# Optimization experiments

Hardware: AMD Instinct MI355X
Metric: run time of the kernel (lower is better)

## Reference

```python
import jax, jax.numpy as jnp
import numpy as np
from jax import lax

K = 3        # kernel_size
PAD = 1      # padding
DIL = 1      # dilation
C_IN = 64
C_OUT = 64
B, H, W = 8, 128, 128


def conv2d(x, w, b, pad):
    # x: [n,c,h,w], w: [o,i,kh,kw], pad: (ph, pw)
    out = lax.conv_general_dilated(
        x, w, window_strides=(1, 1),
        padding=[(pad[0], pad[0]), (pad[1], pad[1])],
        rhs_dilation=(DIL, DIL),
        dimension_numbers=("NCHW", "OIHW", "NCHW"))
    return out + b[None, :, None, None]


def bilinear_sample(x, py, px):
    # x: [n,c,h,w]; py/px: [n,K,h,w] fractional sample coords (zeros outside).
    n, c, h, w = x.shape
    y0 = jnp.floor(py)
    x0 = jnp.floor(px)
    wy = py - y0  # frac weights
    wx = px - x0
    xf = x.reshape(n, c, h * w)

    def gather(yi, xi):
        valid = ((yi >= 0) & (yi < h) & (xi >= 0) & (xi < w)).astype(x.dtype)
        yc = jnp.clip(yi, 0, h - 1).astype(jnp.int32)
        xc = jnp.clip(xi, 0, w - 1).astype(jnp.int32)
        idx = (yc * w + xc).reshape(n, -1)  # [n, K*h*w]
        g = jax.vmap(lambda xb, ib: jnp.take(xb, ib, axis=1))(xf, idx)
        return g.reshape(n, c, *yi.shape[1:]), valid

    v00, m00 = gather(y0, x0)
    v01, m01 = gather(y0, x0 + 1)
    v10, m10 = gather(y0 + 1, x0)
    v11, m11 = gather(y0 + 1, x0 + 1)
    w00 = ((1 - wy) * (1 - wx) * m00)[:, None]
    w01 = ((1 - wy) * wx * m01)[:, None]
    w10 = (wy * (1 - wx) * m10)[:, None]
    w11 = (wy * wx * m11)[:, None]
    return v00 * w00 + v01 * w01 + v10 * w10 + v11 * w11  # [n,c,K,h,w]


def deform_conv_axial(x, offset, mask, w, b, ky_base, kx_base):
    # offset: [n,K,2,h,w] (dy, dx per tap); mask: [n,K,h,w]
    # ky_base/kx_base: [K] static tap displacements
    n, c, h, wd = x.shape
    ii = jnp.arange(h, dtype=x.dtype)[None, None, :, None]
    jj = jnp.arange(wd, dtype=x.dtype)[None, None, None, :]
    py = ii + ky_base[None, :, None, None] + offset[:, :, 0]
    px = jj + kx_base[None, :, None, None] + offset[:, :, 1]
    val = bilinear_sample(x, py, px) * mask[:, None]  # [n,c,K,h,w]
    out = jnp.einsum('nckhw,ock->nohw', val, w.reshape(w.shape[0], c, K))
    return out + b[None, :, None, None]


def setup_inputs() -> dict:
    key = jax.random.key(0)
    ks = jax.random.split(key, 14)
    sc = 0.05
    d = {
        'x': jax.random.normal(ks[0], (B, C_IN, H, W), dtype=jnp.float32),
        'w_off_h': jax.random.normal(ks[1], (2 * K, C_IN, 1, K), dtype=jnp.float32) * sc,
        'b_off_h': jnp.zeros((2 * K,), dtype=jnp.float32),
        'w_mask_h': jax.random.normal(ks[2], (K, C_IN, 1, K), dtype=jnp.float32) * sc,
        'b_mask_h': jnp.zeros((K,), dtype=jnp.float32),
        'w_off_v': jax.random.normal(ks[3], (2 * K, C_IN, K, 1), dtype=jnp.float32) * sc,
        'b_off_v': jnp.zeros((2 * K,), dtype=jnp.float32),
        'w_mask_v': jax.random.normal(ks[4], (K, C_IN, K, 1), dtype=jnp.float32) * sc,
        'b_mask_v': jnp.zeros((K,), dtype=jnp.float32),
        'w_h': jax.random.normal(ks[5], (C_OUT, C_IN, 1, K), dtype=jnp.float32) * (1.0 / np.sqrt(C_IN * K)),
        'b_h': jax.random.normal(ks[6], (C_OUT,), dtype=jnp.float32) * 0.01,
        'w_v': jax.random.normal(ks[7], (C_OUT, C_OUT, K, 1), dtype=jnp.float32) * (1.0 / np.sqrt(C_OUT * K)),
        'b_v': jax.random.normal(ks[8], (C_OUT,), dtype=jnp.float32) * 0.01,
    }
    return d


def reference(x, w_off_h, b_off_h, w_mask_h, b_mask_h, w_off_v, b_off_v,
              w_mask_v, b_mask_v, w_h, b_h, w_v, b_v):
    n, c, h, w = x.shape
    taps = jnp.arange(K, dtype=x.dtype) * DIL - PAD  # [-1,0,1] for K=3,pad=1
    zeros_k = jnp.zeros((K,), dtype=x.dtype)

    # Horizontal pass: offsets/masks from x, deformable (1,K) conv on x
    offset_h = conv2d(x, w_off_h, b_off_h, (0, PAD)).reshape(n, K, 2, h, w)
    mask_h = jax.nn.sigmoid(conv2d(x, w_mask_h, b_mask_h, (0, PAD)))  # [n,K,h,w]
    x_h = deform_conv_axial(x, offset_h, mask_h, w_h, b_h, zeros_k, taps)

    # Vertical pass: offsets/masks from x, deformable (K,1) conv on x_h
    offset_v = conv2d(x, w_off_v, b_off_v, (PAD, 0)).reshape(n, K, 2, h, w)
    mask_v = jax.nn.sigmoid(conv2d(x, w_mask_v, b_mask_v, (PAD, 0)))
    x_v = deform_conv_axial(x_h, offset_v, mask_v, w_v, b_v, taps, zeros_k)
    return x_v
```

## Files before the change

### kernel.cpp

```cpp
#include <hip/hip_runtime.h>

#define C_ 64
#define H_ 128
#define W_ 128
#define B_ 8
#define HW_ (H_*W_)
#define NPIX (B_*HW_)

typedef _Float16 half8 __attribute__((ext_vector_type(8)));
typedef _Float16 half4 __attribute__((ext_vector_type(4)));
typedef float floatx4 __attribute__((ext_vector_type(4)));

__global__ __launch_bounds__(256) void prep_kernel(
    const float* __restrict__ w_off_h, const float* __restrict__ w_mask_h,
    const float* __restrict__ w_off_v, const float* __restrict__ w_mask_v,
    const float* __restrict__ w_h, const float* __restrict__ w_v,
    float* __restrict__ wOffAll, _Float16* __restrict__ wF16_h,
    _Float16* __restrict__ wF16_v)
{
    int gid = blockIdx.x * 256 + threadIdx.x;
    if (gid < 64 * 56) {
        int c = gid / 56, idx = gid - 56 * c;
        float v = 0.f;
        if (idx < 18)      v = w_off_h [((idx      ) / 3) * 192 + c * 3 + (idx      ) % 3];
        else if (idx < 27) v = w_mask_h[((idx - 18) / 3) * 192 + c * 3 + (idx - 18) % 3];
        else if (idx < 45) v = w_off_v [((idx - 27) / 3) * 192 + c * 3 + (idx - 27) % 3];
        else if (idx < 54) v = w_mask_v[((idx - 45) / 3) * 192 + c * 3 + (idx - 45) % 3];
        wOffAll[c * 56 + idx] = v;
    } else if (gid < 3584 + 24576) {
        int i = gid - 3584;
        if (i < 12288) wF16_h[i] = (_Float16)w_h[i];
        else           wF16_v[i - 12288] = (_Float16)w_v[i - 12288];
    }
}

__global__ __launch_bounds__(256, 8) void transpose_kernel(
    const float* __restrict__ x, _Float16* __restrict__ xT)
{
    __shared__ _Float16 tile[64][66];
    int lane = threadIdx.x & 63;
    int wv   = threadIdx.x >> 6;
    int bid = blockIdx.x;
    int n = bid & 7;
    int m = bid >> 3;
    const float* xs = x + (size_t)n * C_ * HW_ + (size_t)m * 64;
    #pragma unroll
    for (int cc = 0; cc < 16; ++cc) {
        int c = wv * 16 + cc;
        tile[c][lane] = (_Float16)xs[(size_t)c * HW_ + lane];
    }
    __syncthreads();
    _Float16* xd = xT + ((size_t)n * HW_ + (size_t)m * 64) * 64;
    #pragma unroll
    for (int pp = 0; pp < 16; ++pp) {
        int p = wv * 16 + pp;
        xd[(size_t)p * 64 + lane] = tile[lane][p];
    }
}

#define SWIZZLE_NP()                        \
    int bid = blockIdx.x;                   \
    int n   = bid & 7;                      \
    int m   = bid >> 3;       \
    int pix = m * 64 + lane;                \
    int j = pix & (W_ - 1);                 \
    int i = pix >> 7;

#define TAP_SETUP_192(OFFP, MASKP, KYO, KXO)                                  \
    {                                                                         \
        int t = threadIdx.x;                                                  \
        if (t < 192) {                                                        \
            int p = t / 3, k = t - 3 * p;                                     \
            int pixp = m * 64 + p;                                            \
            float dy = (OFFP##_DY);                                           \
            float dx = (OFFP##_DX);                                           \
            float mm = (MASKP);                                               \
            float fi = (float)(pixp >> 7), fj = (float)(pixp & (W_ - 1));     \
            float py = fi + (float)(KYO) + dy;                                \
            float px = fj + (float)(KXO) + dx;                                \
            float y0f = floorf(py), x0f = floorf(px);                         \
            float wy = py - y0f, wx = px - x0f;                               \
            int y0 = (int)y0f, x0 = (int)x0f;                                 \
            int y1 = y0 + 1, x1 = x0 + 1;                                     \
            bool vy0 = (y0 >= 0) && (y0 < H_);                                \
            bool vy1 = (y1 >= 0) && (y1 < H_);                                \
            bool vx0 = (x0 >= 0) && (x0 < W_);                                \
            bool vx1 = (x1 >= 0) && (x1 < W_);                                \
            int y0c = min(max(y0, 0), H_ - 1), y1c = min(max(y1, 0), H_ - 1); \
            int x0c = min(max(x0, 0), W_ - 1), x1c = min(max(x1, 0), W_ - 1); \
            float wy1 = 1.f - wy, wx1 = 1.f - wx;                             \
            floatx4 w;                                                        \
            w[0] = (vy0 && vx0) ? wy1 * wx1 * mm : 0.f;                       \
            w[1] = (vy0 && vx1) ? wy1 * wx  * mm : 0.f;                       \
            w[2] = (vy1 && vx0) ? wy  * wx1 * mm : 0.f;                       \
            w[3] = (vy1 && vx1) ? wy  * wx  * mm : 0.f;                       \
            int4 e;                                                           \
            e.x = (y0c * W_ + x0c) * 64;                                      \
            e.y = (y0c * W_ + x1c) * 64;                                      \
            e.z = (y1c * W_ + x0c) * 64;                                      \
            e.w = (y1c * W_ + x1c) * 64;                                      \
            tapI[t] = e;                                                      \
            tapW[t] = w;                                                      \
        }                                                                     \
    }

#define GATHER_MFMA_BODY(ST)                                                  \
    int col = lane & 15;                                                      \
    floatx4 accT[4];                                                          \
    _Pragma("unroll")                                                         \
    for (int T = 0; T < 4; ++T) accT[T] = floatx4{0.f, 0.f, 0.f, 0.f};        \
    _Pragma("unroll")                                                         \
    for (int hf = 0; hf < 2; ++hf) {                                          \
        _Pragma("unroll")                                                     \
        for (int q = 0; q < 8; ++q) {                                         \
            int r = wv * 8 + q;                                               \
            int p = hf * 32 + r;                                              \
            _Pragma("unroll")                                                 \
            for (int k = 0; k < 3; ++k) {                                     \
                int4 e = tapI[p * 3 + k];                                     \
                floatx4 w = tapW[p * 3 + k];                                  \
                float v00 = (float)(ST)[e.x + lane];                          \
                float v01 = (float)(ST)[e.y + lane];                          \
                float v10 = (float)(ST)[e.z + lane];                          \
                float v11 = (float)(ST)[e.w + lane];                          \
                float v = fmaf(w[0], v00, fmaf(w[1], v01,                     \
                          fmaf(w[2], v10, w[3] * v11)));                      \
                valT[r][3 * lane + k] = (_Float16)v;                          \
            }                                                                 \
        }                                                                     \
        __syncthreads();                                                      \
        const _Float16* wpA = wF16 + (size_t)(c0 + (lane & 15)) * 192         \
                            + ((lane >> 4) << 3);                             \
        half8 A0 = *((const half8*)(wpA +   0));                              \
        half8 A1 = *((const half8*)(wpA +  32));                              \
        half8 A2 = *((const half8*)(wpA +  64));                              \
        half8 A3 = *((const half8*)(wpA +  96));                              \
        half8 A4 = *((const half8*)(wpA + 128));                              \
        half8 A5 = *((const half8*)(wpA + 160));                              \
        _Pragma("unroll")                                                     \
        for (int tt = 0; tt < 2; ++tt) {                                      \
            int T = hf * 2 + tt;                                              \
            const _Float16* bp = &valT[tt * 16 + col][(lane >> 4) << 3];      \
            floatx4 acc = accT[T];                                            \
            acc = __builtin_amdgcn_mfma_f32_16x16x32_f16(A0, *((const half8*)(bp +   0)), acc, 0, 0, 0); \
            acc = __builtin_amdgcn_mfma_f32_16x16x32_f16(A1, *((const half8*)(bp +  32)), acc, 0, 0, 0); \
            acc = __builtin_amdgcn_mfma_f32_16x16x32_f16(A2, *((const half8*)(bp +  64)), acc, 0, 0, 0); \
            acc = __builtin_amdgcn_mfma_f32_16x16x32_f16(A3, *((const half8*)(bp +  96)), acc, 0, 0, 0); \
            acc = __builtin_amdgcn_mfma_f32_16x16x32_f16(A4, *((const half8*)(bp + 128)), acc, 0, 0, 0); \
            acc = __builtin_amdgcn_mfma_f32_16x16x32_f16(A5, *((const half8*)(bp + 160)), acc, 0, 0, 0); \
            accT[T] = acc;                                                    \
        }                                                                     \
        if (hf == 0) __syncthreads();                                         \
    }

__global__ __launch_bounds__(256, 8) void deform_h_kernel(
    const float* __restrict__ x, const _Float16* __restrict__ xT,
    const float* __restrict__ wOffAll,
    const float* __restrict__ b_off_h, const float* __restrict__ b_mask_h,
    const float* __restrict__ b_off_v, const float* __restrict__ b_mask_v,
    const _Float16* __restrict__ wF16, const float* __restrict__ bias,
    float* __restrict__ off_v, float* __restrict__ mask_v,
    _Float16* __restrict__ x_hT)
{
    __shared__ __align__(16) char smem[18944];
    float (*red)[18][64] = reinterpret_cast<float(*)[18][64]>(smem);
    float (*red0)[64]    = reinterpret_cast<float(*)[64]>(smem);
    _Float16 (*valT)[200] = reinterpret_cast<_Float16(*)[200]>(smem);
    int4*    tapI = reinterpret_cast<int4*>(smem + 12800);
    floatx4* tapW = reinterpret_cast<floatx4*>(smem + 12800 + 3072);

    int lane = threadIdx.x & 63;
    int wv   = threadIdx.x >> 6;
    int c0 = __builtin_amdgcn_readfirstlane(wv << 4);

    SWIZZLE_NP();

    float a[18];
    #pragma unroll
    for (int o = 0; o < 18; ++o) a[o] = 0.f;

    const float* xs = x + (size_t)n * C_ * HW_ + (size_t)c0 * HW_;
    for (int cc = 0; cc < 16; ++cc) {
        const float* s = xs + cc * HW_;
        float xc = s[pix];
        float xl = (j > 0)      ? s[pix - 1]  : 0.f;
        float xr = (j < W_ - 1) ? s[pix + 1]  : 0.f;
        float xu = (i > 0)      ? s[pix - W_] : 0.f;
        float xd = (i < H_ - 1) ? s[pix + W_] : 0.f;
        const float* wc = wOffAll + (c0 + cc) * 56;
        #pragma unroll
        for (int o = 0; o < 6; ++o) {
            a[o]   = fmaf(xl, wc[3*o],    fmaf(xc, wc[3*o+1],    fmaf(xr, wc[3*o+2],    a[o])));
            a[9+o] = fmaf(xu, wc[27+3*o], fmaf(xc, wc[27+3*o+1], fmaf(xd, wc[27+3*o+2], a[9+o])));
        }
        #pragma unroll
        for (int o = 0; o < 3; ++o) {
            a[6+o]  = fmaf(xl, wc[18+3*o], fmaf(xc, wc[18+3*o+1], fmaf(xr, wc[18+3*o+2], a[6+o])));
            a[15+o] = fmaf(xu, wc[45+3*o], fmaf(xc, wc[45+3*o+1], fmaf(xd, wc[45+3*o+2], a[15+o])));
        }
    }

    #pragma unroll
    for (int o = 0; o < 18; ++o) red[wv][o][lane] = a[o];
    __syncthreads();

    for (int v = threadIdx.x; v < 18 * 64; v += 256) {
        int idx = v >> 6;
        int px  = v & 63;
        float sum = red[0][idx][px] + red[1][idx][px]
                  + red[2][idx][px] + red[3][idx][px];
        int pixg = m * 64 + px;
        if (idx < 6) {
            red[0][idx][px] = sum + b_off_h[idx];
        } else if (idx < 9) {
            red[0][idx][px] = 1.f / (1.f + __expf(-(sum + b_mask_h[idx - 6])));
        } else if (idx < 15) {
            off_v[((size_t)n * 6 + (idx - 9)) * HW_ + pixg] = sum + b_off_v[idx - 9];
        } else {
            mask_v[((size_t)n * 3 + (idx - 15)) * HW_ + pixg] =
                1.f / (1.f + __expf(-(sum + b_mask_v[idx - 15])));
        }
    }
    __syncthreads();

#define H_DY red0[2*k    ][p]
#define H_DX red0[2*k + 1][p]
    TAP_SETUP_192(H, red0[6 + k][p], 0, (k - 1))
#undef H_DY
#undef H_DX
    __syncthreads();

    const _Float16* sT = xT + (size_t)n * (HW_ * 64);
    GATHER_MFMA_BODY(sT)

    int orow = c0 + ((lane >> 4) << 2);
    floatx4 bv = *((const floatx4*)&bias[orow]);
    _Float16* hb = x_hT + ((size_t)n * HW_ + (size_t)m * 64) * 64 + orow;
    #pragma unroll
    for (int T = 0; T < 4; ++T) {
        half4 o;
        o[0] = (_Float16)(accT[T][0] + bv[0]);
        o[1] = (_Float16)(accT[T][1] + bv[1]);
        o[2] = (_Float16)(accT[T][2] + bv[2]);
        o[3] = (_Float16)(accT[T][3] + bv[3]);
        *((half4*)(hb + (size_t)(T * 16 + col) * 64)) = o;
    }
}

__global__ __launch_bounds__(256, 8) void deform_v_kernel(
    const _Float16* __restrict__ srcT, const float* __restrict__ off,
    const float* __restrict__ mask, const _Float16* __restrict__ wF16,
    const float* __restrict__ bias, float* __restrict__ out)
{
    __shared__ __align__(16) char smem[18944];
    _Float16 (*valT)[200] = reinterpret_cast<_Float16(*)[200]>(smem);
    int4*    tapI = reinterpret_cast<int4*>(smem + 12800);
    floatx4* tapW = reinterpret_cast<floatx4*>(smem + 12800 + 3072);

    int lane = threadIdx.x & 63;
    int wv   = threadIdx.x >> 6;
    int c0 = __builtin_amdgcn_readfirstlane(wv << 4);

    int bid = blockIdx.x;
    int n   = bid & 7;
    int m   = bid >> 3;

#define V_DY off[(((size_t)n * 3 + k) * 2 + 0) * HW_ + pixp]
#define V_DX off[(((size_t)n * 3 + k) * 2 + 1) * HW_ + pixp]
    TAP_SETUP_192(V, mask[((size_t)n * 3 + k) * HW_ + pixp], (k - 1), 0)
#undef V_DY
#undef V_DX
    __syncthreads();

    const _Float16* sT = srcT + (size_t)n * (HW_ * 64);
    GATHER_MFMA_BODY(sT)

    int orow = c0 + ((lane >> 4) << 2);
    floatx4 bv = *((const floatx4*)&bias[orow]);
    float* ob = out + ((size_t)n * C_ + orow) * HW_ + m * 64 + col;
    #pragma unroll
    for (int T = 0; T < 4; ++T) {
        __builtin_nontemporal_store(accT[T][0] + bv[0], &ob[T * 16 + (size_t)0 * HW_]);
        __builtin_nontemporal_store(accT[T][1] + bv[1], &ob[T * 16 + (size_t)1 * HW_]);
        __builtin_nontemporal_store(accT[T][2] + bv[2], &ob[T * 16 + (size_t)2 * HW_]);
        __builtin_nontemporal_store(accT[T][3] + bv[3], &ob[T * 16 + (size_t)3 * HW_]);
    }
}

extern "C" void kernel_launch(void* const* d_in, const int* in_sizes, int n_in,
                              void* d_out, int out_size, void* d_ws, size_t ws_size,
                              hipStream_t stream)
{
    const float* x        = (const float*)d_in[0];
    const float* w_off_h  = (const float*)d_in[1];
    const float* b_off_h  = (const float*)d_in[2];
    const float* w_mask_h = (const float*)d_in[3];
    const float* b_mask_h = (const float*)d_in[4];
    const float* w_off_v  = (const float*)d_in[5];
    const float* b_off_v  = (const float*)d_in[6];
    const float* w_mask_v = (const float*)d_in[7];
    const float* b_mask_v = (const float*)d_in[8];
    const float* w_h      = (const float*)d_in[9];
    const float* b_h      = (const float*)d_in[10];
    const float* w_v      = (const float*)d_in[11];
    const float* b_v      = (const float*)d_in[12];

    float* ws      = (float*)d_ws;
    float* off_v   = ws;
    float* mask_v  = off_v  + 786432;
    float* wOffAll = mask_v + 393216;
    _Float16* xT     = (_Float16*)(wOffAll + 3584);
    _Float16* x_hT   = xT + 8388608;
    _Float16* wF16_h = x_hT + 8388608;
    _Float16* wF16_v = wF16_h + 12288;

    prep_kernel<<<110, 256, 0, stream>>>(
        w_off_h, w_mask_h, w_off_v, w_mask_v, w_h, w_v,
        wOffAll, wF16_h, wF16_v);

    dim3 grid(NPIX / 64), block(256);
    transpose_kernel<<<grid, block, 0, stream>>>(x, xT);

    deform_h_kernel<<<grid, block, 0, stream>>>(
        x, xT, wOffAll, b_off_h, b_mask_h, b_off_v, b_mask_v,
        wF16_h, b_h, off_v, mask_v, x_hT);

    deform_v_kernel<<<grid, block, 0, stream>>>(
        x_hT, off_v, mask_v, wF16_v, b_v, (float*)d_out);
}
```

Before: 195.5 us.

## Use single clamped base index per tap with remapped bilinear weights and k-major layout

Each tap now stores one base index: the top-left corner of a 2x2 window clamped to stay inside the image. The four bilinear weights are remapped onto that window's corners, so the four gathers become fixed offsets from one scalar address obtained with readfirstlane. The shared value tile and the fp16 conv weights are reordered from channel-interleaved (3*c+k) to k-major (k*64+c), which gives contiguous LDS writes. This cuts per-tap LDS index storage and vector address arithmetic, at the cost of extra select logic in tap setup and a correctness dependency on the weight remapping at image borders.

```diff
diff --git a/kernel.cpp b/kernel.cpp
--- a/kernel.cpp
+++ b/kernel.cpp
@@ -29,8 +29,16 @@
         wOffAll[c * 56 + idx] = v;
     } else if (gid < 3584 + 24576) {
         int i = gid - 3584;
-        if (i < 12288) wF16_h[i] = (_Float16)w_h[i];
-        else           wF16_v[i - 12288] = (_Float16)w_v[i - 12288];
+        if (i < 12288) {
+            int o = i / 192, rem = i - o * 192;
+            int c = rem / 3, k = rem - 3 * c;
+            wF16_h[o * 192 + k * 64 + c] = (_Float16)w_h[i];
+        } else {
+            i -= 12288;
+            int o = i / 192, rem = i - o * 192;
+            int c = rem / 3, k = rem - 3 * c;
+            wF16_v[o * 192 + k * 64 + c] = (_Float16)w_v[i];
+        }
     }
 }
 
@@ -86,20 +94,26 @@
             bool vy1 = (y1 >= 0) && (y1 < H_);                                \
             bool vx0 = (x0 >= 0) && (x0 < W_);                                \
             bool vx1 = (x1 >= 0) && (x1 < W_);                                \
+            float wy1 = 1.f - wy, wx1 = 1.f - wx;                             \
+            float w00 = (vy0 && vx0) ? wy1 * wx1 * mm : 0.f;                  \
+            float w01 = (vy0 && vx1) ? wy1 * wx  * mm : 0.f;                  \
+            float w10 = (vy1 && vx0) ? wy  * wx1 * mm : 0.f;                  \
+            float w11 = (vy1 && vx1) ? wy  * wx  * mm : 0.f;                  \
             int y0c = min(max(y0, 0), H_ - 1), y1c = min(max(y1, 0), H_ - 1); \
             int x0c = min(max(x0, 0), W_ - 1), x1c = min(max(x1, 0), W_ - 1); \
-            float wy1 = 1.f - wy, wx1 = 1.f - wx;                             \
+            int yb = min(max(y0, 0), H_ - 2),  xb = min(max(x0, 0), W_ - 2);  \
+            int r0 = y0c - yb, r1 = y1c - yb;                   \
+            int cA = x0c - xb, cB = x1c - xb;                   \
             floatx4 w;                                                        \
-            w[0] = (vy0 && vx0) ? wy1 * wx1 * mm : 0.f;                       \
-            w[1] = (vy0 && vx1) ? wy1 * wx  * mm : 0.f;                       \
-            w[2] = (vy1 && vx0) ? wy  * wx1 * mm : 0.f;                       \
-            w[3] = (vy1 && vx1) ? wy  * wx  * mm : 0.f;                       \
-            int4 e;                                                           \
-            e.x = (y0c * W_ + x0c) * 64;                                      \
-            e.y = (y0c * W_ + x1c) * 64;                                      \
-            e.z = (y1c * W_ + x0c) * 64;                                      \
-            e.w = (y1c * W_ + x1c) * 64;                                      \
-            tapI[t] = e;                                                      \
+            w[0] = ((r0==0)&&(cA==0)?w00:0.f) + ((r0==0)&&(cB==0)?w01:0.f)    \
+                 + ((r1==0)&&(cA==0)?w10:0.f) + ((r1==0)&&(cB==0)?w11:0.f);   \
+            w[1] = ((r0==0)&&(cA==1)?w00:0.f) + ((r0==0)&&(cB==1)?w01:0.f)    \
+                 + ((r1==0)&&(cA==1)?w10:0.f) + ((r1==0)&&(cB==1)?w11:0.f);   \
+            w[2] = ((r0==1)&&(cA==0)?w00:0.f) + ((r0==1)&&(cB==0)?w01:0.f)    \
+                 + ((r1==1)&&(cA==0)?w10:0.f) + ((r1==1)&&(cB==0)?w11:0.f);   \
+            w[3] = ((r0==1)&&(cA==1)?w00:0.f) + ((r0==1)&&(cB==1)?w01:0.f)    \
+                 + ((r1==1)&&(cA==1)?w10:0.f) + ((r1==1)&&(cB==1)?w11:0.f);   \
+            tapI[t] = (yb * W_ + xb) * 64;                                    \
             tapW[t] = w;                                                      \
         }                                                                     \
     }
@@ -117,15 +131,16 @@
             int p = hf * 32 + r;                                              \
             _Pragma("unroll")                                                 \
             for (int k = 0; k < 3; ++k) {                                     \
-                int4 e = tapI[p * 3 + k];                                     \
+                int ex = __builtin_amdgcn_readfirstlane(tapI[p * 3 + k]);     \
                 floatx4 w = tapW[p * 3 + k];                                  \
-                float v00 = (float)(ST)[e.x + lane];                          \
-                float v01 = (float)(ST)[e.y + lane];                          \
-                float v10 = (float)(ST)[e.z + lane];                          \
-                float v11 = (float)(ST)[e.w + lane];                          \
+                const _Float16* cb = (ST) + ex;                               \
+                float v00 = (float)cb[lane];                                  \
+                float v01 = (float)cb[lane + 64];                             \
+                float v10 = (float)cb[lane + 64 * W_];                        \
+                float v11 = (float)cb[lane + 64 * W_ + 64];                   \
                 float v = fmaf(w[0], v00, fmaf(w[1], v01,                     \
                           fmaf(w[2], v10, w[3] * v11)));                      \
-                valT[r][3 * lane + k] = (_Float16)v;                          \
+                valT[r][k * 64 + lane] = (_Float16)v;                         \
             }                                                                 \
         }                                                                     \
         __syncthreads();                                                      \
@@ -162,12 +177,12 @@
     float* __restrict__ off_v, float* __restrict__ mask_v,
     _Float16* __restrict__ x_hT)
 {
-    __shared__ __align__(16) char smem[18944];
+    __shared__ __align__(16) char smem[18432];
     float (*red)[18][64] = reinterpret_cast<float(*)[18][64]>(smem);
     float (*red0)[64]    = reinterpret_cast<float(*)[64]>(smem);
     _Float16 (*valT)[200] = reinterpret_cast<_Float16(*)[200]>(smem);
-    int4*    tapI = reinterpret_cast<int4*>(smem + 12800);
-    floatx4* tapW = reinterpret_cast<floatx4*>(smem + 12800 + 3072);
+    int*     tapI = reinterpret_cast<int*>(smem + 12800);
+    floatx4* tapW = reinterpret_cast<floatx4*>(smem + 13568);
 
     int lane = threadIdx.x & 63;
     int wv   = threadIdx.x >> 6;
@@ -252,10 +267,10 @@
     const float* __restrict__ mask, const _Float16* __restrict__ wF16,
     const float* __restrict__ bias, float* __restrict__ out)
 {
-    __shared__ __align__(16) char smem[18944];
+    __shared__ __align__(16) char smem[16640];
     _Float16 (*valT)[200] = reinterpret_cast<_Float16(*)[200]>(smem);
-    int4*    tapI = reinterpret_cast<int4*>(smem + 12800);
-    floatx4* tapW = reinterpret_cast<floatx4*>(smem + 12800 + 3072);
+    int*     tapI = reinterpret_cast<int*>(smem + 12800);
+    floatx4* tapW = reinterpret_cast<floatx4*>(smem + 13568);
 
     int lane = threadIdx.x & 63;
     int wv   = threadIdx.x >> 6;
```

New measurement: 190.3 us. -2.6%, faster.
